# Kernel tuning notes

Measured on AMD Instinct MI355X. Metric: run time of the kernel, lower is better.

## Reference

```python
import jax, jax.numpy as jnp
import numpy as np

T_STEPS = 64   # number of actions (T-1 in the torch code)
BATCH = 512
STATE = 256
ACTION = 64
BELIEF = 1024
HIDDEN = 1024
EMB = 1024
MIN_STD = 0.1


def setup_inputs() -> dict:
    key = jax.random.key(0)
    ks = jax.random.split(key, 16)
    def w(k, shape):
        return jax.random.normal(k, shape, jnp.float32) * 0.02
    return {
        "s_0": jax.random.normal(ks[0], (BATCH, STATE), jnp.float32),
        "A": jax.random.normal(ks[1], (T_STEPS, BATCH, ACTION), jnp.float32),
        "b_0": jax.random.normal(ks[2], (BATCH, BELIEF), jnp.float32),
        "O": jax.random.normal(ks[3], (T_STEPS, BATCH, EMB), jnp.float32),
        "M": jnp.ones((T_STEPS, BATCH, 1), jnp.float32),
        "noise_pri": jax.random.normal(ks[4], (T_STEPS, BATCH, STATE), jnp.float32),
        "noise_pos": jax.random.normal(ks[5], (T_STEPS, BATCH, STATE), jnp.float32),
        # learned parameters (torch nn.Linear convention: y = x @ W.T + b)
        "W_sa": w(ks[6], (BELIEF, STATE + ACTION)), "b_sa": jnp.zeros((BELIEF,), jnp.float32),
        "W_ih": w(ks[7], (3 * BELIEF, BELIEF)), "b_ih": jnp.zeros((3 * BELIEF,), jnp.float32),
        "W_hh": w(ks[8], (3 * BELIEF, BELIEF)), "b_hh": jnp.zeros((3 * BELIEF,), jnp.float32),
        "W_bpri": w(ks[9], (HIDDEN, BELIEF)), "b_bpri": jnp.zeros((HIDDEN,), jnp.float32),
        "W_spri": w(ks[10], (2 * STATE, HIDDEN)), "b_spri": jnp.zeros((2 * STATE,), jnp.float32),
        "W_bpos": w(ks[11], (HIDDEN, BELIEF + EMB)), "b_bpos": jnp.zeros((HIDDEN,), jnp.float32),
        "W_spos": w(ks[12], (2 * STATE, HIDDEN)), "b_spos": jnp.zeros((2 * STATE,), jnp.float32),
    }


def reference(s_0, A, b_0, O, M, noise_pri, noise_pos,
              W_sa, b_sa, W_ih, b_ih, W_hh, b_hh,
              W_bpri, b_bpri, W_spri, b_spri,
              W_bpos, b_bpos, W_spos, b_spos):
    act = jax.nn.relu  # cfg.activation_function = 'relu'

    def gru_cell(x, h):
        # torch GRUCell gate order: r, z, n
        gi = x @ W_ih.T + b_ih      # [B, 3*BELIEF]
        gh = h @ W_hh.T + b_hh
        i_r, i_z, i_n = jnp.split(gi, 3, axis=1)
        h_r, h_z, h_n = jnp.split(gh, 3, axis=1)
        r = jax.nn.sigmoid(i_r + h_r)
        z = jax.nn.sigmoid(i_z + h_z)
        n = jnp.tanh(i_n + r * h_n)
        return (1.0 - z) * n + z * h

    def step(carry, xs):
        b, s = carry  # belief [B,BELIEF], posterior state [B,STATE]
        a_t, o_t, m_t, eps_p, eps_q = xs
        s_in = s * m_t  # non-terminal mask
        x = act(jnp.concatenate([s_in, a_t], axis=1) @ W_sa.T + b_sa)
        b_new = gru_cell(x, b)
        # prior
        pri = act(b_new @ W_bpri.T + b_bpri) @ W_spri.T + b_spri
        mu_p, hp = jnp.split(pri, 2, axis=1)
        std_p = jax.nn.softplus(hp) + MIN_STD
        s_p = mu_p + std_p * eps_p
        # posterior (uses current observation embedding)
        pos = act(jnp.concatenate([b_new, o_t], axis=1) @ W_bpos.T + b_bpos) @ W_spos.T + b_spos
        mu_q, hq = jnp.split(pos, 2, axis=1)
        std_q = jax.nn.softplus(hq) + MIN_STD
        s_q = mu_q + std_q * eps_q
        return (b_new, s_q), (b_new, s_p, mu_p, std_p, s_q, mu_q, std_q)

    (_, _), ys = jax.lax.scan(step, (b_0, s_0), (A, O, M, noise_pri, noise_pos))
    B_out, S_pri, MU_pri, STD_pri, S_pos, MU_pos, STD_pos = ys
    return B_out, S_pri, MU_pri, STD_pri, S_pos, MU_pos, STD_pos
```

## Files before the change

### kernel.cpp

```cpp
#include <hip/hip_runtime.h>
#include <hip/hip_bf16.h>
#include <math.h>

typedef short bf16x8 __attribute__((ext_vector_type(8)));
typedef float f32x4 __attribute__((ext_vector_type(4)));
typedef unsigned short u16;

#define NT 64
#define NB 512
#define NS 256
#define NA 64
#define NBEL 1024

#define OUT_B      0
#define OUT_SPRI   33554432
#define OUT_MUPRI  41943040
#define OUT_STDPRI 50331648
#define OUT_SPOS   58720256
#define OUT_MUPOS  67108864
#define OUT_STDPOS 75497472

__device__ __forceinline__ f32x4 mfma16(bf16x8 a, bf16x8 b, f32x4 c) {
  return __builtin_amdgcn_mfma_f32_16x16x32_bf16(a, b, c, 0, 0, 0);
}

__device__ __forceinline__ u16 f2bf(float f) {
  union { float f; unsigned u; } v; v.f = f;
  return (u16)((v.u + 0x7FFFu + ((v.u >> 16) & 1u)) >> 16);
}
__device__ __forceinline__ float bf2f(u16 h) {
  union { unsigned u; float f; } v; v.u = ((unsigned)h) << 16; return v.f;
}

__device__ __forceinline__ bf16x8 ld8bf(const u16* p) { return *(const bf16x8*)p; }

__device__ __forceinline__ bf16x8 cvt8(const float* p) {
  const float4 lo = *(const float4*)p;
  const float4 hi = *(const float4*)(p + 4);
  bf16x8 v;
  v[0] = (short)f2bf(lo.x); v[1] = (short)f2bf(lo.y);
  v[2] = (short)f2bf(lo.z); v[3] = (short)f2bf(lo.w);
  v[4] = (short)f2bf(hi.x); v[5] = (short)f2bf(hi.y);
  v[6] = (short)f2bf(hi.z); v[7] = (short)f2bf(hi.w);
  return v;
}

__device__ __forceinline__ float sigm(float x) { return 1.f / (1.f + __expf(-x)); }
__device__ __forceinline__ float softplus_(float x) {
  if (x > 20.f) return x;
  return log1pf(__expf(x));
}

#define ZACC(acc) { acc[0][0] = (f32x4){0.f,0.f,0.f,0.f}; acc[0][1] = (f32x4){0.f,0.f,0.f,0.f}; \
                    acc[1][0] = (f32x4){0.f,0.f,0.f,0.f}; acc[1][1] = (f32x4){0.f,0.f,0.f,0.f}; }

#define Q4(acc, a0v, a1v, b0v, b1v) \
  acc[0][0] = mfma16(a0v, b0v, acc[0][0]); \
  acc[0][1] = mfma16(a0v, b1v, acc[0][1]); \
  acc[1][0] = mfma16(a1v, b0v, acc[1][0]); \
  acc[1][1] = mfma16(a1v, b1v, acc[1][1]);

__device__ __forceinline__ void gtile(f32x4 (&acc)[2][2],
    const u16* __restrict__ A, int lda, const u16* __restrict__ B, int ldb,
    int K, int r16, int kq) {
  const u16* A0 = A + r16 * lda + kq * 8;
  const u16* A1 = A0 + 16 * lda;
  const u16* B0 = B + (size_t)r16 * ldb + kq * 8;
  const u16* B1 = B0 + 16 * ldb;
#pragma unroll 4
  for (int k = 0; k < K; k += 32) {
    bf16x8 a0 = ld8bf(A0 + k), a1 = ld8bf(A1 + k);
    bf16x8 b0 = ld8bf(B0 + k), b1 = ld8bf(B1 + k);
    Q4(acc, a0, a1, b0, b1);
  }
}
__device__ __forceinline__ void gtileF(f32x4 (&acc)[2][2],
    const float* __restrict__ A, int lda, const u16* __restrict__ B, int ldb,
    int K, int r16, int kq) {
  const float* A0 = A + r16 * lda + kq * 8;
  const float* A1 = A0 + 16 * lda;
  const u16* B0 = B + (size_t)r16 * ldb + kq * 8;
  const u16* B1 = B0 + 16 * ldb;
#pragma unroll 2
  for (int k = 0; k < K; k += 32) {
    bf16x8 a0 = cvt8(A0 + k), a1 = cvt8(A1 + k);
    bf16x8 b0 = ld8bf(B0 + k), b1 = ld8bf(B1 + k);
    Q4(acc, a0, a1, b0, b1);
  }
}

__device__ __forceinline__ void red_write(float* L, f32x4 (&acc)[2][2], int l) {
  const int base = l * 16;
#pragma unroll
  for (int i = 0; i < 2; ++i)
#pragma unroll
    for (int j = 0; j < 2; ++j)
#pragma unroll
      for (int q = 0; q < 4; ++q)
        L[base + (i * 2 + j) * 4 + q] = acc[i][j][q];
}
__device__ __forceinline__ void red_add(const float* L, f32x4 (&acc)[2][2], int l) {
  const int base = l * 16;
#pragma unroll
  for (int i = 0; i < 2; ++i)
#pragma unroll
    for (int j = 0; j < 2; ++j)
#pragma unroll
      for (int q = 0; q < 4; ++q)
        acc[i][j][q] += L[base + (i * 2 + j) * 4 + q];
}

__device__ __forceinline__ void setflag_blk(unsigned* f) {
  __syncthreads();
  if (threadIdx.x == 0)
    __hip_atomic_fetch_add(f, 1u, __ATOMIC_RELEASE, __HIP_MEMORY_SCOPE_AGENT);
}
__device__ __forceinline__ void waitflag_blk(unsigned* f, unsigned target) {
  if (threadIdx.x == 0) {
    while (__hip_atomic_load(f, __ATOMIC_RELAXED, __HIP_MEMORY_SCOPE_AGENT) < target)
      __builtin_amdgcn_s_sleep(2);
    (void)__hip_atomic_load(f, __ATOMIC_ACQUIRE, __HIP_MEMORY_SCOPE_AGENT);
  }
  __syncthreads();
}

__global__ __launch_bounds__(256) void cvt_weights_k(
    const float* __restrict__ wsa, const float* __restrict__ wih,
    const float* __restrict__ whh, const float* __restrict__ wbpri,
    const float* __restrict__ wspri, const float* __restrict__ wbpos,
    const float* __restrict__ wspos, u16* __restrict__ dst) {
  const int S0 = 327680;
  const int S1 = S0 + 3145728;
  const int S2 = S1 + 3145728;
  const int S3 = S2 + 1048576;
  const int S4 = S3 + 524288;
  const int S5 = S4 + 2097152;
  const int S6 = S5 + 524288;
  for (int i = blockIdx.x * blockDim.x + threadIdx.x; i < S6;
       i += gridDim.x * blockDim.x) {
    float v;
    if (i < S0) v = wsa[i];
    else if (i < S1) v = wih[i - S0];
    else if (i < S2) v = whh[i - S1];
    else if (i < S3) v = wbpri[i - S2];
    else if (i < S4) v = wspri[i - S3];
    else if (i < S5) v = wbpos[i - S4];
    else v = wspos[i - S5];
    dst[i] = f2bf(v);
  }
}

__global__ __launch_bounds__(256) void init_carry_k(
    const float* __restrict__ s0, const float* __restrict__ b0,
    const float* __restrict__ Mptr, u16* __restrict__ smask,
    u16* __restrict__ bbf, float* __restrict__ hf,
    unsigned* __restrict__ flags) {
  for (int i = blockIdx.x * blockDim.x + threadIdx.x; i < NB * NBEL;
       i += gridDim.x * blockDim.x) {
    float b = b0[i];
    bbf[i] = f2bf(b);
    hf[i] = b;
    if (i < NB * NS) {
      int row = i >> 8;
      smask[i] = f2bf(s0[i] * Mptr[row]);
    }
    if (i < 2048) flags[i] = 0;
  }
}


__device__ __forceinline__ void dev_spri(
    int g, int wid, int kh, int r16, int kq, int l, int tt,
    const u16* __restrict__ hpri, const u16* __restrict__ wspri,
    const float* __restrict__ bspri, const float* __restrict__ npri,
    float* __restrict__ out, float* lred0, float* lred1) {
  const int bm = g >> 2, bn = g & 3;
  const int row0 = bm * 64 + (wid >> 1) * 32;
  const int c0 = bn * 64 + (wid & 1) * 32;
  f32x4 am[2][2], ah[2][2];
  ZACC(am); ZACC(ah);
  const u16* A0 = hpri + (row0 + r16) * NBEL + kh * 512 + kq * 8;
  const u16* A1 = A0 + 16 * NBEL;
  const u16* Bm0 = wspri + (size_t)(c0 + r16) * NBEL + kh * 512 + kq * 8;
  const u16* Bm1 = Bm0 + 16 * NBEL;
  const u16* Bh0 = wspri + (size_t)(c0 + 256 + r16) * NBEL + kh * 512 + kq * 8;
  const u16* Bh1 = Bh0 + 16 * NBEL;
#pragma unroll 4
  for (int k = 0; k < 512; k += 32) {
    bf16x8 a0 = ld8bf(A0 + k), a1 = ld8bf(A1 + k);
    bf16x8 m0 = ld8bf(Bm0 + k), m1 = ld8bf(Bm1 + k);
    Q4(am, a0, a1, m0, m1);
    bf16x8 h0 = ld8bf(Bh0 + k), h1 = ld8bf(Bh1 + k);
    Q4(ah, a0, a1, h0, h1);
  }
  if (kh == 1) {
    red_write(lred0, am, l);
    red_write(lred1, ah, l);
  }
  __syncthreads();
  if (kh == 0) {
    red_add(lred0, am, l);
    red_add(lred1, ah, l);
#pragma unroll
    for (int i = 0; i < 2; ++i)
#pragma unroll
      for (int j = 0; j < 2; ++j)
#pragma unroll
        for (int q = 0; q < 4; ++q) {
          const int row = row0 + i * 16 + kq * 4 + q;
          const int c = c0 + j * 16 + r16;
          const size_t idx = (size_t)tt * (NB * NS) + (size_t)row * NS + c;
          const float mu = am[i][j][q] + bspri[c];
          const float hp = ah[i][j][q] + bspri[c + 256];
          const float sd = softplus_(hp) + 0.1f;
          out[OUT_SPRI + idx] = mu + sd * npri[idx];
          out[OUT_MUPRI + idx] = mu;
          out[OUT_STDPRI + idx] = sd;
        }
  }
}

__device__ __forceinline__ void dev_x64(
    int g, int wid8, int r16, int kq, int t,
    const u16* __restrict__ smask, const float* __restrict__ Af,
    const u16* __restrict__ wsa, const float* __restrict__ bsa,
    u16* __restrict__ xg) {
  const int row0 = (g >> 3) * 64 + (wid8 >> 2) * 32;
  const int col0 = (g & 7) * 128 + (wid8 & 3) * 32;
  f32x4 acc[2][2]; ZACC(acc);
  gtile(acc, smask + row0 * NS, NS, wsa + (size_t)col0 * 320, 320, 256, r16, kq);
  gtileF(acc, Af + (size_t)t * (NB * NA) + (size_t)row0 * NA, NA,
         wsa + (size_t)col0 * 320 + 256, 320, 64, r16, kq);
#pragma unroll
  for (int i = 0; i < 2; ++i)
#pragma unroll
    for (int j = 0; j < 2; ++j)
#pragma unroll
      for (int q = 0; q < 4; ++q) {
        const int row = row0 + i * 16 + kq * 4 + q;
        const int col = col0 + j * 16 + r16;
        xg[row * NBEL + col] = f2bf(fmaxf(acc[i][j][q] + bsa[col], 0.f));
      }
}

__device__ __forceinline__ void dev_hbO64(
    int g, int wid8, int r16, int kq,
    const float* __restrict__ OfT, const u16* __restrict__ wbpos,
    float* __restrict__ hbOn) {
  const int row0 = (g >> 3) * 64 + (wid8 >> 2) * 32;
  const int col0 = (g & 7) * 128 + (wid8 & 3) * 32;
  f32x4 acc[2][2]; ZACC(acc);
  gtileF(acc, OfT + (size_t)row0 * NBEL, NBEL,
         wbpos + (size_t)col0 * 2048 + 1024, 2048, 1024, r16, kq);
#pragma unroll
  for (int i = 0; i < 2; ++i)
#pragma unroll
    for (int j = 0; j < 2; ++j)
#pragma unroll
      for (int q = 0; q < 4; ++q) {
        const int row = row0 + i * 16 + kq * 4 + q;
        const int col = col0 + j * 16 + r16;
        hbOn[row * NBEL + col] = acc[i][j][q];
      }
}

__device__ __forceinline__ void dev_gh96(
    int g, int wid8, int r16, int kq,
    const u16* __restrict__ bsrc, const u16* __restrict__ whh,
    const float* __restrict__ bhh, u16* __restrict__ ghn) {
  const int bm = g / 12, bc = g % 12;
  const int row0 = bm * 64 + (wid8 >> 2) * 32;
#pragma unroll
  for (int jt = 0; jt < 2; ++jt) {
    const int col0 = bc * 256 + (wid8 & 3) * 32 + jt * 128;
    f32x4 acc[2][2]; ZACC(acc);
    gtile(acc, bsrc + row0 * NBEL, NBEL, whh + (size_t)col0 * NBEL, NBEL,
          1024, r16, kq);
#pragma unroll
    for (int i = 0; i < 2; ++i)
#pragma unroll
      for (int j = 0; j < 2; ++j)
#pragma unroll
        for (int q = 0; q < 4; ++q) {
          const int row = row0 + i * 16 + kq * 4 + q;
          const int col = col0 + j * 16 + r16;
          ghn[row * 3072 + col] = f2bf(acc[i][j][q] + bhh[col]);
        }
  }
}

__device__ __forceinline__ void dev_bpri64(
    int g, int wid8, int r16, int kq,
    const u16* __restrict__ bcur, const u16* __restrict__ wbpri,
    const float* __restrict__ bbpri, u16* __restrict__ hpri) {
  const int row0 = (g >> 3) * 64 + (wid8 >> 2) * 32;
  const int col0 = (g & 7) * 128 + (wid8 & 3) * 32;
  f32x4 acc[2][2]; ZACC(acc);
  gtile(acc, bcur + row0 * NBEL, NBEL, wbpri + (size_t)col0 * NBEL, NBEL,
        1024, r16, kq);
#pragma unroll
  for (int i = 0; i < 2; ++i)
#pragma unroll
    for (int j = 0; j < 2; ++j)
#pragma unroll
      for (int q = 0; q < 4; ++q) {
        const int row = row0 + i * 16 + kq * 4 + q;
        const int col = col0 + j * 16 + r16;
        hpri[row * NBEL + col] = f2bf(fmaxf(acc[i][j][q] + bbpri[col], 0.f));
      }
}

__global__ __launch_bounds__(512, 2) void kX0(
    const u16* __restrict__ smask, const float* __restrict__ Af,
    const u16* __restrict__ wsa, const float* __restrict__ bsa,
    u16* __restrict__ xg, const float* __restrict__ Of,
    const u16* __restrict__ wbpos, float* __restrict__ hbO0,
    const u16* __restrict__ bbf, const u16* __restrict__ whh,
    const float* __restrict__ bhh, u16* __restrict__ ghA) {
  const int l = threadIdx.x & 63, r16 = l & 15, kq = l >> 4;
  const int wid8 = threadIdx.x >> 6;
  if (blockIdx.x < 64) {
    dev_x64(blockIdx.x, wid8, r16, kq, 0, smask, Af, wsa, bsa, xg);
  } else if (blockIdx.x < 128) {
    dev_hbO64(blockIdx.x - 64, wid8, r16, kq, Of, wbpos, hbO0);
  } else {
    dev_gh96(blockIdx.x - 128, wid8, r16, kq, bbf, whh, bhh, ghA);
  }
}

__global__ __launch_bounds__(512, 2) void kG(
    const u16* __restrict__ xg, const u16* __restrict__ wih,
    const float* __restrict__ bih, const u16* __restrict__ ghc,
    float* __restrict__ hf, u16* __restrict__ bcur, float* __restrict__ out,
    const u16* __restrict__ hpriPrev, const u16* __restrict__ wspri,
    const float* __restrict__ bspri, const float* __restrict__ npri,
    const float* __restrict__ Of, const u16* __restrict__ wbpos,
    float* __restrict__ hbOn, int t) {
  __shared__ float lred[4][3][1024];
  const int l = threadIdx.x & 63, r16 = l & 15, kq = l >> 4;
  const int wid8 = threadIdx.x >> 6;
  const int wid = wid8 & 3, kh = wid8 >> 2;
  if (blockIdx.x < 128) {
    const int g = blockIdx.x, bm = g >> 4, bn = g & 15;
    const int row0 = bm * 64 + (wid >> 1) * 32;
    const int col0 = bn * 64 + (wid & 1) * 32;
    f32x4 ar[2][2], az[2][2], an[2][2];
    ZACC(ar); ZACC(az); ZACC(an);
    const u16* A0 = xg + (row0 + r16) * NBEL + kh * 512 + kq * 8;
    const u16* A1 = A0 + 16 * NBEL;
    const u16* Br0 = wih + (size_t)(col0 + r16) * NBEL + kh * 512 + kq * 8;
    const u16* Br1 = Br0 + 16 * NBEL;
    const u16* Bz0 = wih + (size_t)(col0 + 1024 + r16) * NBEL + kh * 512 + kq * 8;
    const u16* Bz1 = Bz0 + 16 * NBEL;
    const u16* Bn0 = wih + (size_t)(col0 + 2048 + r16) * NBEL + kh * 512 + kq * 8;
    const u16* Bn1 = Bn0 + 16 * NBEL;
#pragma unroll 4
    for (int k = 0; k < 512; k += 32) {
      bf16x8 a0 = ld8bf(A0 + k), a1 = ld8bf(A1 + k);
      bf16x8 b0 = ld8bf(Br0 + k), b1 = ld8bf(Br1 + k);
      Q4(ar, a0, a1, b0, b1);
      bf16x8 c0 = ld8bf(Bz0 + k), c1 = ld8bf(Bz1 + k);
      Q4(az, a0, a1, c0, c1);
      bf16x8 d0 = ld8bf(Bn0 + k), d1 = ld8bf(Bn1 + k);
      Q4(an, a0, a1, d0, d1);
    }
    if (kh == 1) {
      red_write(&lred[wid][0][0], ar, l);
      red_write(&lred[wid][1][0], az, l);
      red_write(&lred[wid][2][0], an, l);
    }
    __syncthreads();
    if (kh == 0) {
      const int base = l * 16;
#pragma unroll
      for (int i = 0; i < 2; ++i)
#pragma unroll
        for (int j = 0; j < 2; ++j)
#pragma unroll
          for (int q = 0; q < 4; ++q) {
            const int row = row0 + i * 16 + kq * 4 + q;
            const int c = col0 + j * 16 + r16;
            const int li = base + (i * 2 + j) * 4 + q;
            const u16* ghrow = ghc + row * 3072;
            const float r = sigm(ar[i][j][q] + lred[wid][0][li] + bih[c] +
                                 bf2f(ghrow[c]));
            const float z = sigm(az[i][j][q] + lred[wid][1][li] + bih[c + 1024] +
                                 bf2f(ghrow[c + 1024]));
            const float n = tanhf(an[i][j][q] + lred[wid][2][li] + bih[c + 2048] +
                                  r * bf2f(ghrow[c + 2048]));
            const float h = hf[row * NBEL + c];
            const float bnew = (1.f - z) * n + z * h;
            hf[row * NBEL + c] = bnew;
            bcur[row * NBEL + c] = f2bf(bnew);
            out[OUT_B + (size_t)t * (NB * NBEL) + row * NBEL + c] = bnew;
          }
    }
  } else if (blockIdx.x < 160) {
    if (t >= 1)
      dev_spri(blockIdx.x - 128, wid, kh, r16, kq, l, t - 1,
               hpriPrev, wspri, bspri, npri, out,
               &lred[wid][0][0], &lred[wid][1][0]);
  } else {
    if (t + 1 < NT)
      dev_hbO64(blockIdx.x - 160, wid8, r16, kq,
                Of + (size_t)(t + 1) * (NB * NBEL), wbpos, hbOn);
  }
}

__global__ __launch_bounds__(512, 2) void kM(
    const u16* __restrict__ bcur, const u16* __restrict__ wbpos,
    const float* __restrict__ bbpos, const float* __restrict__ hbOc,
    u16* __restrict__ hbbf,
    const u16* __restrict__ wbpri, const float* __restrict__ bbpri,
    u16* __restrict__ hpriCur,
    const u16* __restrict__ whh, const float* __restrict__ bhh,
    u16* __restrict__ ghn,
    const u16* __restrict__ wspos, const float* __restrict__ bspos,
    const float* __restrict__ npos, const float* __restrict__ Mptr,
    u16* __restrict__ smask,
    const float* __restrict__ Af, const u16* __restrict__ wsa,
    const float* __restrict__ bsa, u16* __restrict__ xg,
    const u16* __restrict__ wspri, const float* __restrict__ bspri,
    const float* __restrict__ npri,
    float* __restrict__ out,
    unsigned* __restrict__ fH8, unsigned* __restrict__ fS8,
    unsigned* __restrict__ fB, int t) {
  __shared__ float lred[4][2][1024];
  const int l = threadIdx.x & 63, r16 = l & 15, kq = l >> 4;
  const int wid8 = threadIdx.x >> 6;
  const int wid = wid8 & 3, kh = wid8 >> 2;
  if (blockIdx.x < 128) {
    const int g = blockIdx.x, bm = g >> 4, bn = g & 15;
    const int row0 = bm * 64 + (wid >> 1) * 32;
    const int col0 = bn * 64 + (wid & 1) * 32;
    f32x4 acc[2][2]; ZACC(acc);
    const u16* A0 = bcur + (row0 + r16) * NBEL + kh * 512 + kq * 8;
    const u16* A1 = A0 + 16 * NBEL;
    const u16* B0 = wbpos + (size_t)(col0 + r16) * 2048 + kh * 512 + kq * 8;
    const u16* B1 = B0 + 16 * 2048;
#pragma unroll 4
    for (int k = 0; k < 512; k += 32) {
      bf16x8 a0 = ld8bf(A0 + k), a1 = ld8bf(A1 + k);
      bf16x8 b0 = ld8bf(B0 + k), b1 = ld8bf(B1 + k);
      Q4(acc, a0, a1, b0, b1);
    }
    if (kh == 1) red_write(&lred[wid][0][0], acc, l);
    __syncthreads();
    if (kh == 0) {
      red_add(&lred[wid][0][0], acc, l);
#pragma unroll
      for (int i = 0; i < 2; ++i)
#pragma unroll
        for (int j = 0; j < 2; ++j)
#pragma unroll
          for (int q = 0; q < 4; ++q) {
            const int row = row0 + i * 16 + kq * 4 + q;
            const int col = col0 + j * 16 + r16;
            const float v = acc[i][j][q] + hbOc[row * NBEL + col] + bbpos[col];
            hbbf[row * NBEL + col] = f2bf(fmaxf(v, 0.f));
          }
    }
    setflag_blk(fH8 + t * 8 + bm);
  } else if (blockIdx.x < 192) {
    dev_bpri64(blockIdx.x - 128, wid8, r16, kq, bcur, wbpri, bbpri, hpriCur);
    setflag_blk(fB + t);
  } else if (blockIdx.x < 288) {
    if (t + 1 < NT)
      dev_gh96(blockIdx.x - 192, wid8, r16, kq, bcur, whh, bhh, ghn);
  } else if (blockIdx.x < 320) {
    const int g = blockIdx.x - 288, bm = g >> 2, bn = g & 3;
    waitflag_blk(fH8 + t * 8 + bm, 16);
    const int row0 = bm * 64 + (wid >> 1) * 32;
    const int c0 = bn * 64 + (wid & 1) * 32;
    f32x4 am[2][2], ah[2][2];
    ZACC(am); ZACC(ah);
    const u16* A0 = hbbf + (row0 + r16) * NBEL + kh * 512 + kq * 8;
    const u16* A1 = A0 + 16 * NBEL;
    const u16* Bm0 = wspos + (size_t)(c0 + r16) * NBEL + kh * 512 + kq * 8;
    const u16* Bm1 = Bm0 + 16 * NBEL;
    const u16* Bh0 = wspos + (size_t)(c0 + 256 + r16) * NBEL + kh * 512 + kq * 8;
    const u16* Bh1 = Bh0 + 16 * NBEL;
#pragma unroll 4
    for (int k = 0; k < 512; k += 32) {
      bf16x8 a0 = ld8bf(A0 + k), a1 = ld8bf(A1 + k);
      bf16x8 m0 = ld8bf(Bm0 + k), m1 = ld8bf(Bm1 + k);
      Q4(am, a0, a1, m0, m1);
      bf16x8 h0 = ld8bf(Bh0 + k), h1 = ld8bf(Bh1 + k);
      Q4(ah, a0, a1, h0, h1);
    }
    if (kh == 1) {
      red_write(&lred[wid][0][0], am, l);
      red_write(&lred[wid][1][0], ah, l);
    }
    __syncthreads();
    if (kh == 0) {
      red_add(&lred[wid][0][0], am, l);
      red_add(&lred[wid][1][0], ah, l);
#pragma unroll
      for (int i = 0; i < 2; ++i)
#pragma unroll
        for (int j = 0; j < 2; ++j)
#pragma unroll
          for (int q = 0; q < 4; ++q) {
            const int row = row0 + i * 16 + kq * 4 + q;
            const int c = c0 + j * 16 + r16;
            const float mu = am[i][j][q] + bspos[c];
            const float hq = ah[i][j][q] + bspos[c + 256];
            const float sd = softplus_(hq) + 0.1f;
            const size_t idx = (size_t)t * (NB * NS) + (size_t)row * NS + c;
            const float sq = mu + sd * npos[idx];
            out[OUT_SPOS + idx] = sq;
            out[OUT_MUPOS + idx] = mu;
            out[OUT_STDPOS + idx] = sd;
            const float mn = (t < NT - 1) ? Mptr[(t + 1) * NB + row] : 1.f;
            smask[row * NS + c] = f2bf(sq * mn);
          }
    }
    setflag_blk(fS8 + t * 8 + bm);
  } else if (blockIdx.x < 384) {
    if (t + 1 >= NT) return;
    const int g = blockIdx.x - 320;
    waitflag_blk(fS8 + t * 8 + (g >> 3), 4);
    dev_x64(g, wid8, r16, kq, t + 1, smask, Af, wsa, bsa, xg);
  } else {
    if (t != NT - 1) return;
    waitflag_blk(fB + t, 64);
    dev_spri(blockIdx.x - 384, wid, kh, r16, kq, l, t,
             hpriCur, wspri, bspri, npri, out,
             &lred[wid][0][0], &lred[wid][1][0]);
  }
}

extern "C" void kernel_launch(void* const* d_in, const int* in_sizes, int n_in,
                              void* d_out, int out_size, void* d_ws, size_t ws_size,
                              hipStream_t stream) {
  const float* s0 = (const float*)d_in[0];
  const float* Af = (const float*)d_in[1];
  const float* b0 = (const float*)d_in[2];
  const float* Of = (const float*)d_in[3];
  const float* Mp = (const float*)d_in[4];
  const float* npri = (const float*)d_in[5];
  const float* npos = (const float*)d_in[6];
  const float* Wsa = (const float*)d_in[7];
  const float* bsa = (const float*)d_in[8];
  const float* Wih = (const float*)d_in[9];
  const float* bih = (const float*)d_in[10];
  const float* Whh = (const float*)d_in[11];
  const float* bhh = (const float*)d_in[12];
  const float* Wbpri = (const float*)d_in[13];
  const float* bbpri = (const float*)d_in[14];
  const float* Wspri = (const float*)d_in[15];
  const float* bspri = (const float*)d_in[16];
  const float* Wbpos = (const float*)d_in[17];
  const float* bbpos = (const float*)d_in[18];
  const float* Wspos = (const float*)d_in[19];
  const float* bspos = (const float*)d_in[20];

  float* out = (float*)d_out;
  char* ws = (char*)d_ws;
  u16* wbase   = (u16*)ws;
  u16* wsa_b   = wbase;
  u16* wih_b   = wbase + 327680;
  u16* whh_b   = wbase + 3473408;
  u16* wbpri_b = wbase + 6619136;
  u16* wspri_b = wbase + 7667712;
  u16* wbpos_b = wbase + 8192000;
  u16* wspos_b = wbase + 10289152;
  u16*   smask = (u16*)  (ws + 21626880);
  u16*   bbf   = (u16*)  (ws + 21889024);
  float* hf    = (float*)(ws + 22937600);
  u16*   xg    = (u16*)  (ws + 25034752);
  float* hbO0  = (float*)(ws + 26083328);
  float* hbO1  = (float*)(ws + 28180480);
  u16*   hbbf  = (u16*)  (ws + 30277632);
  u16*   hpri0 = (u16*)  (ws + 31326208);
  u16*   hpri1 = (u16*)  (ws + 32374784);
  u16*   ghA   = (u16*)  (ws + 33423360);
  u16*   ghB   = (u16*)  (ws + 36569088);
  unsigned* flags = (unsigned*)(ws + 39714816);
  unsigned* fH8 = flags;
  unsigned* fS8 = flags + 512;
  unsigned* fB  = flags + 1024;

  cvt_weights_k<<<2048, 256, 0, stream>>>(Wsa, Wih, Whh, Wbpri, Wspri, Wbpos,
                                          Wspos, wbase);
  init_carry_k<<<2048, 256, 0, stream>>>(s0, b0, Mp, smask, bbf, hf, flags);
  kX0<<<224, 512, 0, stream>>>(smask, Af, wsa_b, bsa, xg, Of, wbpos_b, hbO0,
                               bbf, whh_b, bhh, ghA);

  for (int t = 0; t < NT; ++t) {
    float* hbOc = (t & 1) ? hbO1 : hbO0;
    float* hbOn = (t & 1) ? hbO0 : hbO1;
    u16* ghc = (t & 1) ? ghB : ghA;
    u16* ghn = (t & 1) ? ghA : ghB;
    u16* hpriCur  = (t & 1) ? hpri1 : hpri0;
    u16* hpriPrev = (t & 1) ? hpri0 : hpri1;
    kG<<<224, 512, 0, stream>>>(xg, wih_b, bih, ghc, hf, bbf, out,
                                hpriPrev, wspri_b, bspri, npri,
                                Of, wbpos_b, hbOn, t);
    kM<<<416, 512, 0, stream>>>(bbf, wbpos_b, bbpos, hbOc, hbbf,
                                wbpri_b, bbpri, hpriCur,
                                whh_b, bhh, ghn,
                                wspos_b, bspos, npos, Mp, smask,
                                Af, wsa_b, bsa, xg,
                                wspri_b, bspri, npri,
                                out, fH8, fS8, fB, t);
  }
}
```

Before: 8.095 ms.

## Halve GEMM tile widths in GRU and posterior blocks to double grid parallelism

The GRU input-gate GEMM in kG and the belief-posterior GEMM in kM now use 64x32 tiles instead of 64x64, doubling their block counts to 256. The W_hh precompute is regrouped into 48 larger blocks so the total grid stays modest. Block index ranges and flag wait counts are adjusted to match. The aim is to fill more CUs on the critical-path GEMMs, at the cost of each block reusing its A operand less and so loading more redundantly.

```diff
diff --git a/kernel.cpp b/kernel.cpp
--- a/kernel.cpp
+++ b/kernel.cpp
@@ -289,6 +289,31 @@
   }
 }
 
+__device__ __forceinline__ void dev_gh48(
+    int g, int wid8, int r16, int kq,
+    const u16* __restrict__ bsrc, const u16* __restrict__ whh,
+    const float* __restrict__ bhh, u16* __restrict__ ghn) {
+  const int bm = g / 6, bc = g % 6;
+  const int row0 = bm * 64 + (wid8 >> 2) * 32;
+#pragma unroll
+  for (int jt = 0; jt < 4; ++jt) {
+    const int col0 = bc * 512 + jt * 128 + (wid8 & 3) * 32;
+    f32x4 acc[2][2]; ZACC(acc);
+    gtile(acc, bsrc + row0 * NBEL, NBEL, whh + (size_t)col0 * NBEL, NBEL,
+          1024, r16, kq);
+#pragma unroll
+    for (int i = 0; i < 2; ++i)
+#pragma unroll
+      for (int j = 0; j < 2; ++j)
+#pragma unroll
+        for (int q = 0; q < 4; ++q) {
+          const int row = row0 + i * 16 + kq * 4 + q;
+          const int col = col0 + j * 16 + r16;
+          ghn[row * 3072 + col] = f2bf(acc[i][j][q] + bhh[col]);
+        }
+  }
+}
+
 __device__ __forceinline__ void dev_bpri64(
     int g, int wid8, int r16, int kq,
     const u16* __restrict__ bcur, const u16* __restrict__ wbpri,
@@ -336,73 +361,76 @@
     const float* __restrict__ bspri, const float* __restrict__ npri,
     const float* __restrict__ Of, const u16* __restrict__ wbpos,
     float* __restrict__ hbOn, int t) {
-  __shared__ float lred[4][3][1024];
+  __shared__ float lred[4][2][1024];
   const int l = threadIdx.x & 63, r16 = l & 15, kq = l >> 4;
   const int wid8 = threadIdx.x >> 6;
   const int wid = wid8 & 3, kh = wid8 >> 2;
-  if (blockIdx.x < 128) {
-    const int g = blockIdx.x, bm = g >> 4, bn = g & 15;
+  if (blockIdx.x < 256) {
+    const int g = blockIdx.x, bm = g >> 5, bn = g & 31;
     const int row0 = bm * 64 + (wid >> 1) * 32;
-    const int col0 = bn * 64 + (wid & 1) * 32;
-    f32x4 ar[2][2], az[2][2], an[2][2];
-    ZACC(ar); ZACC(az); ZACC(an);
+    const int col0 = bn * 32 + (wid & 1) * 16;
+    f32x4 ar[2], az[2], an[2];
+    ar[0] = ar[1] = az[0] = az[1] = an[0] = an[1] = (f32x4){0.f, 0.f, 0.f, 0.f};
     const u16* A0 = xg + (row0 + r16) * NBEL + kh * 512 + kq * 8;
     const u16* A1 = A0 + 16 * NBEL;
-    const u16* Br0 = wih + (size_t)(col0 + r16) * NBEL + kh * 512 + kq * 8;
-    const u16* Br1 = Br0 + 16 * NBEL;
-    const u16* Bz0 = wih + (size_t)(col0 + 1024 + r16) * NBEL + kh * 512 + kq * 8;
-    const u16* Bz1 = Bz0 + 16 * NBEL;
-    const u16* Bn0 = wih + (size_t)(col0 + 2048 + r16) * NBEL + kh * 512 + kq * 8;
-    const u16* Bn1 = Bn0 + 16 * NBEL;
+    const u16* Br = wih + (size_t)(col0 + r16) * NBEL + kh * 512 + kq * 8;
+    const u16* Bz = Br + (size_t)1024 * NBEL;
+    const u16* Bn = Br + (size_t)2048 * NBEL;
 #pragma unroll 4
     for (int k = 0; k < 512; k += 32) {
       bf16x8 a0 = ld8bf(A0 + k), a1 = ld8bf(A1 + k);
-      bf16x8 b0 = ld8bf(Br0 + k), b1 = ld8bf(Br1 + k);
-      Q4(ar, a0, a1, b0, b1);
-      bf16x8 c0 = ld8bf(Bz0 + k), c1 = ld8bf(Bz1 + k);
-      Q4(az, a0, a1, c0, c1);
-      bf16x8 d0 = ld8bf(Bn0 + k), d1 = ld8bf(Bn1 + k);
-      Q4(an, a0, a1, d0, d1);
-    }
+      bf16x8 br = ld8bf(Br + k);
+      ar[0] = mfma16(a0, br, ar[0]); ar[1] = mfma16(a1, br, ar[1]);
+      bf16x8 bz = ld8bf(Bz + k);
+      az[0] = mfma16(a0, bz, az[0]); az[1] = mfma16(a1, bz, az[1]);
+      bf16x8 bn_ = ld8bf(Bn + k);
+      an[0] = mfma16(a0, bn_, an[0]); an[1] = mfma16(a1, bn_, an[1]);
+    }
+    float* Lr = &lred[wid][0][0];
+    float* Lz = &lred[wid][0][512];
+    float* Ln = &lred[wid][1][0];
     if (kh == 1) {
-      red_write(&lred[wid][0][0], ar, l);
-      red_write(&lred[wid][1][0], az, l);
-      red_write(&lred[wid][2][0], an, l);
+      const int base = l * 8;
+#pragma unroll
+      for (int i = 0; i < 2; ++i)
+#pragma unroll
+        for (int q = 0; q < 4; ++q) {
+          Lr[base + i * 4 + q] = ar[i][q];
+          Lz[base + i * 4 + q] = az[i][q];
+          Ln[base + i * 4 + q] = an[i][q];
+        }
     }
     __syncthreads();
     if (kh == 0) {
-      const int base = l * 16;
+      const int base = l * 8;
 #pragma unroll
       for (int i = 0; i < 2; ++i)
 #pragma unroll
-        for (int j = 0; j < 2; ++j)
-#pragma unroll
-          for (int q = 0; q < 4; ++q) {
-            const int row = row0 + i * 16 + kq * 4 + q;
-            const int c = col0 + j * 16 + r16;
-            const int li = base + (i * 2 + j) * 4 + q;
-            const u16* ghrow = ghc + row * 3072;
-            const float r = sigm(ar[i][j][q] + lred[wid][0][li] + bih[c] +
-                                 bf2f(ghrow[c]));
-            const float z = sigm(az[i][j][q] + lred[wid][1][li] + bih[c + 1024] +
-                                 bf2f(ghrow[c + 1024]));
-            const float n = tanhf(an[i][j][q] + lred[wid][2][li] + bih[c + 2048] +
-                                  r * bf2f(ghrow[c + 2048]));
-            const float h = hf[row * NBEL + c];
-            const float bnew = (1.f - z) * n + z * h;
-            hf[row * NBEL + c] = bnew;
-            bcur[row * NBEL + c] = f2bf(bnew);
-            out[OUT_B + (size_t)t * (NB * NBEL) + row * NBEL + c] = bnew;
-          }
-    }
-  } else if (blockIdx.x < 160) {
+        for (int q = 0; q < 4; ++q) {
+          const int row = row0 + i * 16 + kq * 4 + q;
+          const int c = col0 + r16;
+          const int li = base + i * 4 + q;
+          const u16* ghrow = ghc + row * 3072;
+          const float r = sigm(ar[i][q] + Lr[li] + bih[c] + bf2f(ghrow[c]));
+          const float z = sigm(az[i][q] + Lz[li] + bih[c + 1024] +
+                               bf2f(ghrow[c + 1024]));
+          const float n = tanhf(an[i][q] + Ln[li] + bih[c + 2048] +
+                                r * bf2f(ghrow[c + 2048]));
+          const float h = hf[row * NBEL + c];
+          const float bnew = (1.f - z) * n + z * h;
+          hf[row * NBEL + c] = bnew;
+          bcur[row * NBEL + c] = f2bf(bnew);
+          out[OUT_B + (size_t)t * (NB * NBEL) + row * NBEL + c] = bnew;
+        }
+    }
+  } else if (blockIdx.x < 288) {
     if (t >= 1)
-      dev_spri(blockIdx.x - 128, wid, kh, r16, kq, l, t - 1,
+      dev_spri(blockIdx.x - 256, wid, kh, r16, kq, l, t - 1,
                hpriPrev, wspri, bspri, npri, out,
                &lred[wid][0][0], &lred[wid][1][0]);
   } else {
     if (t + 1 < NT)
-      dev_hbO64(blockIdx.x - 160, wid8, r16, kq,
+      dev_hbO64(blockIdx.x - 288, wid8, r16, kq,
                 Of + (size_t)(t + 1) * (NB * NBEL), wbpos, hbOn);
   }
 }
@@ -429,47 +457,55 @@
   const int l = threadIdx.x & 63, r16 = l & 15, kq = l >> 4;
   const int wid8 = threadIdx.x >> 6;
   const int wid = wid8 & 3, kh = wid8 >> 2;
-  if (blockIdx.x < 128) {
-    const int g = blockIdx.x, bm = g >> 4, bn = g & 15;
+  if (blockIdx.x < 256) {
+    const int g = blockIdx.x, bm = g >> 5, bn = g & 31;
     const int row0 = bm * 64 + (wid >> 1) * 32;
-    const int col0 = bn * 64 + (wid & 1) * 32;
-    f32x4 acc[2][2]; ZACC(acc);
+    const int col0 = bn * 32 + (wid & 1) * 16;
+    f32x4 acc[2];
+    acc[0] = acc[1] = (f32x4){0.f, 0.f, 0.f, 0.f};
     const u16* A0 = bcur + (row0 + r16) * NBEL + kh * 512 + kq * 8;
     const u16* A1 = A0 + 16 * NBEL;
     const u16* B0 = wbpos + (size_t)(col0 + r16) * 2048 + kh * 512 + kq * 8;
-    const u16* B1 = B0 + 16 * 2048;
 #pragma unroll 4
     for (int k = 0; k < 512; k += 32) {
       bf16x8 a0 = ld8bf(A0 + k), a1 = ld8bf(A1 + k);
-      bf16x8 b0 = ld8bf(B0 + k), b1 = ld8bf(B1 + k);
-      Q4(acc, a0, a1, b0, b1);
-    }
-    if (kh == 1) red_write(&lred[wid][0][0], acc, l);
+      bf16x8 b0 = ld8bf(B0 + k);
+      acc[0] = mfma16(a0, b0, acc[0]);
+      acc[1] = mfma16(a1, b0, acc[1]);
+    }
+    float* L = &lred[wid][0][0];
+    if (kh == 1) {
+      const int base = l * 8;
+#pragma unroll
+      for (int i = 0; i < 2; ++i)
+#pragma unroll
+        for (int q = 0; q < 4; ++q)
+          L[base + i * 4 + q] = acc[i][q];
+    }
     __syncthreads();
     if (kh == 0) {
-      red_add(&lred[wid][0][0], acc, l);
+      const int base = l * 8;
 #pragma unroll
       for (int i = 0; i < 2; ++i)
 #pragma unroll
-        for (int j = 0; j < 2; ++j)
-#pragma unroll
-          for (int q = 0; q < 4; ++q) {
-            const int row = row0 + i * 16 + kq * 4 + q;
-            const int col = col0 + j * 16 + r16;
-            const float v = acc[i][j][q] + hbOc[row * NBEL + col] + bbpos[col];
-            hbbf[row * NBEL + col] = f2bf(fmaxf(v, 0.f));
-          }
+        for (int q = 0; q < 4; ++q) {
+          const int row = row0 + i * 16 + kq * 4 + q;
+          const int col = col0 + r16;
+          const float v = acc[i][q] + L[base + i * 4 + q] +
+                          hbOc[row * NBEL + col] + bbpos[col];
+          hbbf[row * NBEL + col] = f2bf(fmaxf(v, 0.f));
+        }
     }
     setflag_blk(fH8 + t * 8 + bm);
-  } else if (blockIdx.x < 192) {
-    dev_bpri64(blockIdx.x - 128, wid8, r16, kq, bcur, wbpri, bbpri, hpriCur);
+  } else if (blockIdx.x < 320) {
+    dev_bpri64(blockIdx.x - 256, wid8, r16, kq, bcur, wbpri, bbpri, hpriCur);
     setflag_blk(fB + t);
-  } else if (blockIdx.x < 288) {
+  } else if (blockIdx.x < 368) {
     if (t + 1 < NT)
-      dev_gh96(blockIdx.x - 192, wid8, r16, kq, bcur, whh, bhh, ghn);
-  } else if (blockIdx.x < 320) {
-    const int g = blockIdx.x - 288, bm = g >> 2, bn = g & 3;
-    waitflag_blk(fH8 + t * 8 + bm, 16);
+      dev_gh48(blockIdx.x - 320, wid8, r16, kq, bcur, whh, bhh, ghn);
+  } else if (blockIdx.x < 400) {
+    const int g = blockIdx.x - 368, bm = g >> 2, bn = g & 3;
+    waitflag_blk(fH8 + t * 8 + bm, 32);
     const int row0 = bm * 64 + (wid >> 1) * 32;
     const int c0 = bn * 64 + (wid & 1) * 32;
     f32x4 am[2][2], ah[2][2];
@@ -517,15 +553,15 @@
           }
     }
     setflag_blk(fS8 + t * 8 + bm);
-  } else if (blockIdx.x < 384) {
+  } else if (blockIdx.x < 464) {
     if (t + 1 >= NT) return;
-    const int g = blockIdx.x - 320;
+    const int g = blockIdx.x - 400;
     waitflag_blk(fS8 + t * 8 + (g >> 3), 4);
     dev_x64(g, wid8, r16, kq, t + 1, smask, Af, wsa, bsa, xg);
   } else {
     if (t != NT - 1) return;
     waitflag_blk(fB + t, 64);
-    dev_spri(blockIdx.x - 384, wid, kh, r16, kq, l, t,
+    dev_spri(blockIdx.x - 464, wid, kh, r16, kq, l, t,
              hpriCur, wspri, bspri, npri, out,
              &lred[wid][0][0], &lred[wid][1][0]);
   }
@@ -595,10 +631,10 @@
     u16* ghn = (t & 1) ? ghA : ghB;
     u16* hpriCur  = (t & 1) ? hpri1 : hpri0;
     u16* hpriPrev = (t & 1) ? hpri0 : hpri1;
-    kG<<<224, 512, 0, stream>>>(xg, wih_b, bih, ghc, hf, bbf, out,
+    kG<<<352, 512, 0, stream>>>(xg, wih_b, bih, ghc, hf, bbf, out,
                                 hpriPrev, wspri_b, bspri, npri,
                                 Of, wbpos_b, hbOn, t);
-    kM<<<416, 512, 0, stream>>>(bbf, wbpos_b, bbpos, hbOc, hbbf,
+    kM<<<496, 512, 0, stream>>>(bbf, wbpos_b, bbpos, hbOc, hbbf,
                                 wbpri_b, bbpri, hpriCur,
                                 whh_b, bhh, ghn,
                                 wspos_b, bspos, npos, Mp, smask,
```

After: 12.63 ms. 1.56x slower.
